# Kernel tuning notes

Hardware: AMD Instinct MI355X
Metric: run time of the kernel (lower is better)

Reference implementation:

```python
import jax, jax.numpy as jnp
import numpy as np

N_NODES = 50000
N_EDGES = 800000
IN_DIM = 256
OUT_DIM = 256


def setup_inputs() -> dict:
    key = jax.random.key(0)
    k_feat, k_src, k_dst, k_w0, k_w1, k_b = jax.random.split(key, 6)
    feat = jax.random.normal(k_feat, (N_NODES, IN_DIM), dtype=jnp.float32)
    src = jax.random.randint(k_src, (N_EDGES,), 0, N_NODES, dtype=jnp.int64)
    dst = jax.random.randint(k_dst, (N_EDGES,), 0, N_NODES, dtype=jnp.int64)
    # GraphConv weights (Glorot-ish scale) and biases
    W0 = jax.random.normal(k_w0, (IN_DIM, OUT_DIM), dtype=jnp.float32) / np.sqrt(IN_DIM)
    W1 = jax.random.normal(k_w1, (OUT_DIM, OUT_DIM), dtype=jnp.float32) / np.sqrt(OUT_DIM)
    b0 = jnp.zeros((OUT_DIM,), dtype=jnp.float32)
    b1 = jnp.zeros((OUT_DIM,), dtype=jnp.float32)
    # single shared nn.PReLU parameter (torch default init 0.25)
    prelu_a = jnp.asarray(0.25, dtype=jnp.float32)
    return {"feat": feat, "src": src, "dst": dst,
            "W0": W0, "b0": b0, "W1": W1, "b1": b1, "prelu_a": prelu_a}


def _prelu(x, a):
    return jnp.where(x >= 0, x, a * x)


def reference(feat, src, dst, W0, b0, W1, b1, prelu_a):
    N = feat.shape[0]
    ones = jnp.ones((src.shape[0],), dtype=feat.dtype)
    out_deg = jnp.zeros((N,), dtype=feat.dtype).at[src].add(ones)
    in_deg = jnp.zeros((N,), dtype=feat.dtype).at[dst].add(ones)
    # DGL norm='both': clamp degrees to >=1 before rsqrt
    norm_s = jax.lax.rsqrt(jnp.maximum(out_deg, 1.0))[:, None]  # [N,1]
    norm_d = jax.lax.rsqrt(jnp.maximum(in_deg, 1.0))[:, None]   # [N,1]

    def graph_conv(h, W, b):
        # h' = D_in^{-1/2} A (D_out^{-1/2} h) W + b
        msg = (h * norm_s)[src]                                   # [E, d]
        agg = jax.ops.segment_sum(msg, dst, num_segments=N)       # [N, d]
        return (agg * norm_d) @ W + b

    h = _prelu(graph_conv(feat, W0, b0), prelu_a)
    hg = jnp.sum(h, axis=0, keepdims=True)                        # SumPooling [1, d]
    h = _prelu(graph_conv(h, W1, b1), prelu_a)
    hg = jnp.concatenate([hg, jnp.sum(h, axis=0, keepdims=True)], axis=-1)
    return (h, hg)
```

## Files before the change

kernel.cpp:

```cpp
#include <hip/hip_runtime.h>
#include <stdint.h>

#define NN 50000
#define NE 800000
#define DIM 256

#define HB 128
#define HT 512
#define HALF 25000

#define NSLICE 4
#define SCH 64
#define NPB 32
#define ECH 1024

#define GR 64
#define GB ((NN + GR - 1) / GR)

#define SCB 49

typedef __bf16 bf16x8 __attribute__((ext_vector_type(8)));
typedef float f32x4 __attribute__((ext_vector_type(4)));
typedef float f32x2 __attribute__((ext_vector_type(2)));
typedef unsigned u32x4 __attribute__((ext_vector_type(4)));
typedef int i32x4 __attribute__((ext_vector_type(4)));

__device__ __forceinline__ unsigned short f2bf(float f) {
  union { float f; unsigned u; } v; v.f = f;
  unsigned r = v.u + 0x7fffu + ((v.u >> 16) & 1u);
  return (unsigned short)(r >> 16);
}

__device__ __forceinline__ void gload_lds16(const void* g, void* l) {
  __builtin_amdgcn_global_load_lds(
      (const __attribute__((address_space(1))) unsigned*)g,
      (__attribute__((address_space(3))) unsigned*)l, 16, 0, 0);
}

__global__ __launch_bounds__(HT) void hist_kernel(const int* __restrict__ src,
                                                  const int* __restrict__ dst,
                                                  unsigned* __restrict__ Hs,
                                                  unsigned* __restrict__ Hd) {
  __shared__ unsigned lds[HALF];
  const int tid = threadIdx.x;
  const int phase = blockIdx.x >> 7;
  const int b = blockIdx.x & (HB - 1);
  const int* arr = phase ? dst : src;
  unsigned* H = phase ? Hd : Hs;
  for (int w = tid; w < HALF; w += HT) lds[w] = 0u;
  __syncthreads();
  for (int e = b * HT + tid; e < NE; e += HB * HT) {
    unsigned n = (unsigned)arr[e];
    atomicAdd(&lds[n >> 1], 1u << ((n & 1) * 16));
  }
  __syncthreads();
  for (int w = tid; w < HALF; w += HT)
    H[(size_t)b * HALF + w] = lds[w];
}

__global__ __launch_bounds__(512) void reduce_norm_kernel(const unsigned* __restrict__ Hs,
                                                          const unsigned* __restrict__ Hd,
                                                          unsigned* __restrict__ Pd,
                                                          int* __restrict__ in_cnt,
                                                          float* __restrict__ norm_s,
                                                          float* __restrict__ norm_d,
                                                          float* __restrict__ hg,
                                                          int* __restrict__ csum) {
  __shared__ int ws[8];
  const int tid = threadIdx.x;
  const int w = blockIdx.x * 512 + tid;
  if (blockIdx.x == 0) hg[tid] = 0.f;
  unsigned ss = 0, dd = 0;
  if (w < HALF) {
    for (int b = 0; b < HB; ++b) {
      Pd[(size_t)b * HALF + w] = dd;
      ss += Hs[(size_t)b * HALF + w];
      dd += Hd[(size_t)b * HALF + w];
    }
    int n0 = w * 2;
    unsigned s0 = ss & 0xffffu, s1 = ss >> 16;
    unsigned d0 = dd & 0xffffu, d1 = dd >> 16;
    in_cnt[n0] = (int)d0;
    in_cnt[n0 + 1] = (int)d1;
    norm_s[n0] = rsqrtf(fmaxf((float)s0, 1.0f));
    norm_s[n0 + 1] = rsqrtf(fmaxf((float)s1, 1.0f));
    norm_d[n0] = rsqrtf(fmaxf((float)d0, 1.0f));
    norm_d[n0 + 1] = rsqrtf(fmaxf((float)d1, 1.0f));
  }
  int deg = (int)((dd & 0xffffu) + (dd >> 16));
  int lane = tid & 63, wave = tid >> 6;
#pragma unroll
  for (int off = 32; off; off >>= 1) deg += __shfl_down(deg, off, 64);
  if (lane == 0) ws[wave] = deg;
  __syncthreads();
  if (tid == 0) {
    int s = 0;
#pragma unroll
    for (int i = 0; i < 8; ++i) s += ws[i];
    csum[blockIdx.x] = s;
  }
}

__global__ __launch_bounds__(256) void scan_write_kernel(const int* __restrict__ in_cnt,
                                                         const int* __restrict__ csum,
                                                         int* __restrict__ row_ptr) {
  __shared__ int wsum[4];
  int tid = threadIdx.x, lane = tid & 63, wave = tid >> 6;
  int cv = (lane < SCB) ? csum[lane] : 0;
  int cincl = cv;
#pragma unroll
  for (int off = 1; off < 64; off <<= 1) {
    int t = __shfl_up(cincl, off, 64);
    if (lane >= off) cincl += t;
  }
  int myoff = __shfl(cincl, blockIdx.x, 64) - __shfl(cv, blockIdx.x, 64);
  int total = __shfl(cincl, SCB - 1, 64);
  if (blockIdx.x == 0 && tid == 0) row_ptr[NN] = total;

  int i0 = blockIdx.x * 1024 + tid * 4;
  int v[4];
#pragma unroll
  for (int j = 0; j < 4; ++j) {
    int i = i0 + j;
    v[j] = (i < NN) ? in_cnt[i] : 0;
  }
  int tsum = v[0] + v[1] + v[2] + v[3];
  int incl = tsum;
#pragma unroll
  for (int off = 1; off < 64; off <<= 1) {
    int t = __shfl_up(incl, off, 64);
    if (lane >= off) incl += t;
  }
  if (lane == 63) wsum[wave] = incl;
  __syncthreads();
  int woff = 0;
  for (int w = 0; w < wave; ++w) woff += wsum[w];
  int run = myoff + woff + (incl - tsum);
#pragma unroll
  for (int j = 0; j < 4; ++j) {
    int i = i0 + j;
    if (i < NN) row_ptr[i] = run;
    run += v[j];
  }
}

__global__ __launch_bounds__(HT) void fill_kernel(const int* __restrict__ src,
                                                  const int* __restrict__ dst,
                                                  const int* __restrict__ row_ptr,
                                                  const unsigned* __restrict__ Pd,
                                                  int* __restrict__ colx) {
  __shared__ unsigned lds[HALF];
  const int tid = threadIdx.x;
  const int b = blockIdx.x;
  for (int w = tid; w < HALF; w += HT) lds[w] = 0u;
  __syncthreads();
  for (int e = b * HT + tid; e < NE; e += HB * HT) {
    int n = dst[e];
    int sh = (n & 1) * 16;
    unsigned old = atomicAdd(&lds[n >> 1], 1u << sh);
    unsigned rank = (old >> sh) & 0xffffu;
    unsigned pref = (Pd[(size_t)b * HALF + (n >> 1)] >> sh) & 0xffffu;
    colx[row_ptr[n] + (int)pref + (int)rank] = src[e] << 7;
  }
}

__device__ __forceinline__ void swizzleW_body(const float* __restrict__ W,
                                              unsigned short* __restrict__ Wb, int idx) {
  int lane = idx & 63;
  int blk = idx >> 6;
  int kc = blk & 7, nt = blk >> 3;
  int kbase = kc * 32 + (lane >> 4) * 8;
  int col = nt * 16 + (lane & 15);
  ushort4 o0, o1;
  o0.x = f2bf(W[(size_t)(kbase + 0) * DIM + col]);
  o0.y = f2bf(W[(size_t)(kbase + 1) * DIM + col]);
  o0.z = f2bf(W[(size_t)(kbase + 2) * DIM + col]);
  o0.w = f2bf(W[(size_t)(kbase + 3) * DIM + col]);
  o1.x = f2bf(W[(size_t)(kbase + 4) * DIM + col]);
  o1.y = f2bf(W[(size_t)(kbase + 5) * DIM + col]);
  o1.z = f2bf(W[(size_t)(kbase + 6) * DIM + col]);
  o1.w = f2bf(W[(size_t)(kbase + 7) * DIM + col]);
  ((ushort4*)Wb)[idx * 2 + 0] = o0;
  ((ushort4*)Wb)[idx * 2 + 1] = o1;
}

__global__ void prep_kernel(const float* __restrict__ feat, const float* __restrict__ norm_s,
                            unsigned short* __restrict__ featb,
                            const float* __restrict__ W0, unsigned short* __restrict__ Wb0,
                            const float* __restrict__ W1, unsigned short* __restrict__ Wb1) {
  int blk = blockIdx.x;
  if (blk < 12500) {
    int i = blk * 256 + threadIdx.x;
    int node = i >> 6;
    int ch4 = i & 63;
    float s = norm_s[node];
    float4 v = ((const float4*)feat)[i];
    ushort4 o;
    o.x = f2bf(v.x * s); o.y = f2bf(v.y * s); o.z = f2bf(v.z * s); o.w = f2bf(v.w * s);
    int sl = ch4 >> 4;
    int w4 = ch4 & 15;
    ((ushort4*)featb)[(size_t)sl * (NN * 16) + (size_t)node * 16 + w4] = o;
  } else if (blk < 12532) {
    swizzleW_body(W0, Wb0, (blk - 12500) * 256 + threadIdx.x);
  } else {
    swizzleW_body(W1, Wb1, (blk - 12532) * 256 + threadIdx.x);
  }
}

__device__ __forceinline__ void acc_row(f32x2* a, u32x4 p) {
  f32x2 v0 = { __uint_as_float(p.x << 16), __uint_as_float(p.x & 0xffff0000u) };
  a[0] += v0;
  f32x2 v1 = { __uint_as_float(p.y << 16), __uint_as_float(p.y & 0xffff0000u) };
  a[1] += v1;
  f32x2 v2 = { __uint_as_float(p.z << 16), __uint_as_float(p.z & 0xffff0000u) };
  a[2] += v2;
  f32x2 v3 = { __uint_as_float(p.w << 16), __uint_as_float(p.w & 0xffff0000u) };
  a[3] += v3;
}

__global__ __launch_bounds__(256) void agg_kernel(const unsigned short* __restrict__ X,
                                                  unsigned short* __restrict__ agg,
                                                  const int* __restrict__ row_ptr,
                                                  const int* __restrict__ colx,
                                                  const float* __restrict__ norm_d) {
  __shared__ int ecol[ECH];
  const int s = blockIdx.x & (NSLICE - 1);
  const int nb = blockIdx.x >> 2;
  const int tid = threadIdx.x;
  const int grp = tid >> 3;
  const int cl = tid & 7;
  const int node = nb * NPB + grp;

  const int nfirst = nb * NPB;
  const int nlast = (nfirst + NPB < NN) ? (nfirst + NPB) : NN;
  const int estart = row_ptr[nfirst];
  const int eend = row_ptr[nlast];

  int e = 0, end = 0;
  if (node < NN) { e = row_ptr[node]; end = row_ptr[node + 1]; }

  const char* Xp = (const char*)(X + (size_t)s * (NN * SCH));
  const int lsub = cl * 16;

  f32x2 a[4];
#pragma unroll
  for (int j = 0; j < 4; ++j) a[j] = (f32x2){0.f, 0.f};

  const int base0 = estart & ~3;
  for (int base = base0; base < eend; base += ECH) {
    const int lim = (base + ECH < eend) ? (base + ECH) : eend;
    __syncthreads();
    for (int k = base + tid * 4; k < lim; k += 1024) {
      i32x4 v = __builtin_nontemporal_load((const i32x4*)(colx + k));
      *(i32x4*)&ecol[k - base] = v;
    }
    __syncthreads();
    const int hi = (end < lim) ? end : lim;
    for (; e + 8 <= hi; e += 8) {
      int o_[8];
#pragma unroll
      for (int j = 0; j < 8; ++j) o_[j] = ecol[e - base + j];
      u32x4 r_[8];
#pragma unroll
      for (int j = 0; j < 8; ++j)
        r_[j] = *(const u32x4*)(Xp + (size_t)(unsigned)(o_[j] | lsub));
#pragma unroll
      for (int j = 0; j < 8; ++j) acc_row(a, r_[j]);
    }
    if (e + 4 <= hi) {
      int o_[4];
#pragma unroll
      for (int j = 0; j < 4; ++j) o_[j] = ecol[e - base + j];
      u32x4 r_[4];
#pragma unroll
      for (int j = 0; j < 4; ++j)
        r_[j] = *(const u32x4*)(Xp + (size_t)(unsigned)(o_[j] | lsub));
#pragma unroll
      for (int j = 0; j < 4; ++j) acc_row(a, r_[j]);
      e += 4;
    }
    for (; e < hi; ++e) {
      int o0 = ecol[e - base];
      u32x4 r = *(const u32x4*)(Xp + (size_t)(unsigned)(o0 | lsub));
      acc_row(a, r);
    }
  }

  if (node < NN) {
    float nd = norm_d[node];
    u32x4 o;
    o.x = (unsigned)f2bf(a[0].x * nd) | ((unsigned)f2bf(a[0].y * nd) << 16);
    o.y = (unsigned)f2bf(a[1].x * nd) | ((unsigned)f2bf(a[1].y * nd) << 16);
    o.z = (unsigned)f2bf(a[2].x * nd) | ((unsigned)f2bf(a[2].y * nd) << 16);
    o.w = (unsigned)f2bf(a[3].x * nd) | ((unsigned)f2bf(a[3].y * nd) << 16);
    unsigned pcol = (unsigned)(s * 128 + cl * 16) ^ (((unsigned)node & 7u) << 4);
    __builtin_nontemporal_store(o, (u32x4*)((char*)agg + (size_t)node * 512 + pcol));
  }
}

#define FROW 260
__global__ __launch_bounds__(256) void gemm_mfma_kernel(const unsigned short* __restrict__ A,
                                                        const unsigned short* __restrict__ Wb,
                                                        const float* __restrict__ bias,
                                                        const float* __restrict__ prelu_a_ptr,
                                                        const float* __restrict__ norm_s,
                                                        float* __restrict__ C,
                                                        unsigned short* __restrict__ Cb,
                                                        float* __restrict__ hg_part) {
  __shared__ __attribute__((aligned(16))) char Asb[GR * 512];
  int tid = threadIdx.x;
  int r0 = blockIdx.x * GR;
  const char* Ab = (const char*)A;
#pragma unroll
  for (int p = 0; p < 8; ++p) {
    int off = p * 4096 + tid * 16;
    int row = off >> 9;
    int col = off & 511;
    int grow = r0 + row;
    if (grow > NN - 1) grow = NN - 1;
    gload_lds16(Ab + (size_t)grow * 512 + col, Asb + off);
  }
  __syncthreads();

  int wave = tid >> 6, lane = tid & 63;
  int quad = lane >> 4, l16 = lane & 15;

  f32x4 acc[4][4];
#pragma unroll
  for (int mt = 0; mt < 4; ++mt)
#pragma unroll
    for (int nti = 0; nti < 4; ++nti)
      acc[mt][nti] = (f32x4){0.f, 0.f, 0.f, 0.f};

#pragma unroll
  for (int kc = 0; kc < 8; ++kc) {
    bf16x8 a[4], b[4];
#pragma unroll
    for (int mt = 0; mt < 4; ++mt) {
      int row = mt * 16 + l16;
      int c = (kc * 64 + quad * 16) ^ ((row & 7) << 4);
      a[mt] = *(const bf16x8*)(Asb + row * 512 + c);
    }
#pragma unroll
    for (int nti = 0; nti < 4; ++nti) {
      int nt = wave * 4 + nti;
      b[nti] = *(const bf16x8*)(Wb + ((size_t)(nt * 8 + kc) * 64 + lane) * 8);
    }
#pragma unroll
    for (int mt = 0; mt < 4; ++mt)
#pragma unroll
      for (int nti = 0; nti < 4; ++nti)
        acc[mt][nti] = __builtin_amdgcn_mfma_f32_16x16x32_bf16(a[mt], b[nti], acc[mt][nti], 0, 0, 0);
  }

  float pa = *prelu_a_ptr;
  float bv[4], cs[4];
#pragma unroll
  for (int nti = 0; nti < 4; ++nti) {
    bv[nti] = bias[wave * 64 + nti * 16 + l16];
    cs[nti] = 0.f;
  }
#pragma unroll
  for (int mt = 0; mt < 4; ++mt) {
#pragma unroll
    for (int nti = 0; nti < 4; ++nti) {
#pragma unroll
      for (int r = 0; r < 4; ++r) {
        int rowg = r0 + mt * 16 + quad * 4 + r;
        float x = acc[mt][nti][r] + bv[nti];
        x = (x >= 0.f) ? x : pa * x;
        acc[mt][nti][r] = x;
        if (rowg < NN) cs[nti] += x;
      }
    }
  }
#pragma unroll
  for (int nti = 0; nti < 4; ++nti) {
    cs[nti] += __shfl_xor(cs[nti], 16, 64);
    cs[nti] += __shfl_xor(cs[nti], 32, 64);
  }
  if (quad == 0) {
#pragma unroll
    for (int nti = 0; nti < 4; ++nti)
      hg_part[(size_t)blockIdx.x * 256 + wave * 64 + nti * 16 + l16] = cs[nti];
  }

  float* LF = (float*)Asb;
#pragma unroll
  for (int chunk = 0; chunk < 4; ++chunk) {
    __syncthreads();
#pragma unroll
    for (int nti = 0; nti < 4; ++nti) {
      int colw = wave * 64 + nti * 16 + l16;
#pragma unroll
      for (int r = 0; r < 4; ++r)
        LF[(quad * 4 + r) * FROW + colw] = acc[chunk][nti][r];
    }
    __syncthreads();
    int rowbase = r0 + chunk * 16;
    if (C) {
#pragma unroll
      for (int s = 0; s < 4; ++s) {
        int g = s * 256 + tid;
        int row = g >> 6, cg = g & 63;
        int rowg = rowbase + row;
        if (rowg < NN) {
          float4 v = *(const float4*)&LF[row * FROW + cg * 4];
          *(float4*)(C + (size_t)rowg * DIM + cg * 4) = v;
        }
      }
    }
    if (Cb) {
#pragma unroll
      for (int s = 0; s < 2; ++s) {
        int g = s * 256 + tid;
        int row = g >> 5, cg = g & 31;
        int rowg = rowbase + row;
        if (rowg < NN) {
          float ns = norm_s[rowg];
          float4 v0 = *(const float4*)&LF[row * FROW + cg * 8];
          float4 v1 = *(const float4*)&LF[row * FROW + cg * 8 + 4];
          uint4 o;
          o.x = (unsigned)f2bf(v0.x * ns) | ((unsigned)f2bf(v0.y * ns) << 16);
          o.y = (unsigned)f2bf(v0.z * ns) | ((unsigned)f2bf(v0.w * ns) << 16);
          o.z = (unsigned)f2bf(v1.x * ns) | ((unsigned)f2bf(v1.y * ns) << 16);
          o.w = (unsigned)f2bf(v1.z * ns) | ((unsigned)f2bf(v1.w * ns) << 16);
          unsigned short* outp = Cb + (size_t)(cg >> 3) * (NN * SCH)
                               + (size_t)rowg * SCH + (size_t)(cg & 7) * 8;
          *(uint4*)outp = o;
        }
      }
    }
  }
}

__global__ __launch_bounds__(256) void hg_reduce_kernel(const float* __restrict__ hg_part,
                                                        float* __restrict__ hg) {
  const int layer = blockIdx.x >> 3;
  const int chunk = blockIdx.x & 7;
  const int c = threadIdx.x;
  const float* base = hg_part + (size_t)layer * GB * 256;
  const int per = (GB + 7) / 8;
  int b0 = chunk * per;
  int b1 = (b0 + per < GB) ? (b0 + per) : GB;
  float s0 = 0.f, s1 = 0.f, s2 = 0.f, s3 = 0.f;
  int b = b0;
  for (; b + 4 <= b1; b += 4) {
    s0 += base[(size_t)(b + 0) * 256 + c];
    s1 += base[(size_t)(b + 1) * 256 + c];
    s2 += base[(size_t)(b + 2) * 256 + c];
    s3 += base[(size_t)(b + 3) * 256 + c];
  }
  for (; b < b1; ++b) s0 += base[(size_t)b * 256 + c];
  atomicAdd(&hg[layer * 256 + c], (s0 + s1) + (s2 + s3));
}

extern "C" void kernel_launch(void* const* d_in, const int* in_sizes, int n_in,
                              void* d_out, int out_size, void* d_ws, size_t ws_size,
                              hipStream_t stream) {
  const float* feat = (const float*)d_in[0];
  const int* src    = (const int*)d_in[1];
  const int* dst    = (const int*)d_in[2];
  const float* W0   = (const float*)d_in[3];
  const float* b0   = (const float*)d_in[4];
  const float* W1   = (const float*)d_in[5];
  const float* b1   = (const float*)d_in[6];
  const float* pa   = (const float*)d_in[7];

  float* out_h = (float*)d_out;
  float* hg    = out_h + (size_t)NN * DIM;

  char* w = (char*)d_ws;
  int* in_cnt   = (int*)w;        w += (size_t)NN * 4;
  float* norm_s = (float*)w;      w += (size_t)NN * 4;
  float* norm_d = (float*)w;      w += (size_t)NN * 4;
  int* row_ptr  = (int*)w;        w += (size_t)(NN + 16) * 4;
  int* colx     = (int*)w;        w += (size_t)(NE + 4) * 4;
  int* csum     = (int*)w;        w += 64 * 4;
  unsigned short* Wb0 = (unsigned short*)w;  w += (size_t)DIM * DIM * 2;
  unsigned short* Wb1 = (unsigned short*)w;  w += (size_t)DIM * DIM * 2;
  float* hg_part = (float*)w;     w += (size_t)2 * GB * 256 * 4;
  uintptr_t ap = ((uintptr_t)w + 255) & ~(uintptr_t)255;
  unsigned short* featb = (unsigned short*)ap;
  unsigned short* aggb  = featb + (size_t)NN * DIM;
  unsigned* Hs = (unsigned*)featb;
  unsigned* Hd = Hs + (size_t)HB * HALF;
  unsigned* Pd = (unsigned*)aggb;

  const int agg_blocks = NSLICE * ((NN + NPB - 1) / NPB);

  hist_kernel<<<2 * HB, HT, 0, stream>>>(src, dst, Hs, Hd);
  reduce_norm_kernel<<<SCB, 512, 0, stream>>>(Hs, Hd, Pd, in_cnt, norm_s, norm_d, hg, csum);
  prep_kernel<<<12564, 256, 0, stream>>>(feat, norm_s, featb, W0, Wb0, W1, Wb1);
  scan_write_kernel<<<SCB, 256, 0, stream>>>(in_cnt, csum, row_ptr);
  fill_kernel<<<HB, HT, 0, stream>>>(src, dst, row_ptr, Pd, colx);

  agg_kernel<<<agg_blocks, 256, 0, stream>>>(featb, aggb, row_ptr, colx, norm_d);
  gemm_mfma_kernel<<<GB, 256, 0, stream>>>(aggb, Wb0, b0, pa, norm_s,
                                           (float*)nullptr, featb, hg_part);

  agg_kernel<<<agg_blocks, 256, 0, stream>>>(featb, aggb, row_ptr, colx, norm_d);
  gemm_mfma_kernel<<<GB, 256, 0, stream>>>(aggb, Wb1, b1, pa, norm_s,
                                           out_h, (unsigned short*)nullptr, hg_part + (size_t)GB * 256);

  hg_reduce_kernel<<<16, 256, 0, stream>>>(hg_part, hg);
}
```

Before: 303.3 us.

## Build CSR with global atomics and aggregate two node groups per block

Drops the per-block LDS histogram and prefix-reduction path that built a deterministic CSR. In its place, a zero kernel, a global-atomic degree count and a global atomic cursor fill colx with edges in nondeterministic order within each row. The aggregation kernel now handles 64 nodes per block (two per thread group) with a larger edge chunk and a 16-wide unrolled gather. The goal is less preprocessing traffic and better latency hiding in the gather. The cost is heavy global atomic contention, and the summation order is no longer deterministic.

Measured after the change: 379.2 us. 1.25x slower.

```diff
diff --git a/kernel.cpp b/kernel.cpp
--- a/kernel.cpp
+++ b/kernel.cpp
@@ -5,14 +5,10 @@
 #define NE 800000
 #define DIM 256
 
-#define HB 128
-#define HT 512
-#define HALF 25000
-
 #define NSLICE 4
 #define SCH 64
-#define NPB 32
-#define ECH 1024
+#define NPB 64
+#define ECH 2048
 
 #define GR 64
 #define GB ((NN + GR - 1) / GR)
@@ -37,75 +33,63 @@
       (__attribute__((address_space(3))) unsigned*)l, 16, 0, 0);
 }
 
-__global__ __launch_bounds__(HT) void hist_kernel(const int* __restrict__ src,
+__global__ __launch_bounds__(256) void zero_kernel(int* __restrict__ cnt, float* __restrict__ hg) {
+  int i = blockIdx.x * 256 + threadIdx.x;
+  if (i < 2 * NN) cnt[i] = 0;
+  if (i < 512) hg[i] = 0.f;
+}
+
+__global__ __launch_bounds__(256) void deg_kernel(const int* __restrict__ src,
                                                   const int* __restrict__ dst,
-                                                  unsigned* __restrict__ Hs,
-                                                  unsigned* __restrict__ Hd) {
-  __shared__ unsigned lds[HALF];
-  const int tid = threadIdx.x;
-  const int phase = blockIdx.x >> 7;
-  const int b = blockIdx.x & (HB - 1);
-  const int* arr = phase ? dst : src;
-  unsigned* H = phase ? Hd : Hs;
-  for (int w = tid; w < HALF; w += HT) lds[w] = 0u;
+                                                  int* __restrict__ cnt) {
+  int t = blockIdx.x * 256 + threadIdx.x;
+  if (t < NE / 4) {
+    i32x4 s4 = *(const i32x4*)(src + t * 4);
+    i32x4 d4 = *(const i32x4*)(dst + t * 4);
+    atomicAdd(&cnt[s4.x], 1);
+    atomicAdd(&cnt[s4.y], 1);
+    atomicAdd(&cnt[s4.z], 1);
+    atomicAdd(&cnt[s4.w], 1);
+    atomicAdd(&cnt[NN + d4.x], 1);
+    atomicAdd(&cnt[NN + d4.y], 1);
+    atomicAdd(&cnt[NN + d4.z], 1);
+    atomicAdd(&cnt[NN + d4.w], 1);
+  }
+}
+
+__global__ __launch_bounds__(256) void norm_kernel(const int* __restrict__ cnt,
+                                                   float* __restrict__ norm_s,
+                                                   float* __restrict__ norm_d,
+                                                   int* __restrict__ csum) {
+  __shared__ int ws[4];
+  int tid = threadIdx.x;
+  int i0 = blockIdx.x * 1024 + tid * 4;
+  int dsum = 0;
+#pragma unroll
+  for (int j = 0; j < 4; ++j) {
+    int i = i0 + j;
+    if (i < NN) {
+      int s = cnt[i], d = cnt[NN + i];
+      norm_s[i] = rsqrtf(fmaxf((float)s, 1.0f));
+      norm_d[i] = rsqrtf(fmaxf((float)d, 1.0f));
+      dsum += d;
+    }
+  }
+  int lane = tid & 63, wave = tid >> 6;
+#pragma unroll
+  for (int off = 32; off; off >>= 1) dsum += __shfl_down(dsum, off, 64);
+  if (lane == 0) ws[wave] = dsum;
   __syncthreads();
-  for (int e = b * HT + tid; e < NE; e += HB * HT) {
-    unsigned n = (unsigned)arr[e];
-    atomicAdd(&lds[n >> 1], 1u << ((n & 1) * 16));
-  }
-  __syncthreads();
-  for (int w = tid; w < HALF; w += HT)
-    H[(size_t)b * HALF + w] = lds[w];
-}
-
-__global__ __launch_bounds__(512) void reduce_norm_kernel(const unsigned* __restrict__ Hs,
-                                                          const unsigned* __restrict__ Hd,
-                                                          unsigned* __restrict__ Pd,
-                                                          int* __restrict__ in_cnt,
-                                                          float* __restrict__ norm_s,
-                                                          float* __restrict__ norm_d,
-                                                          float* __restrict__ hg,
-                                                          int* __restrict__ csum) {
-  __shared__ int ws[8];
-  const int tid = threadIdx.x;
-  const int w = blockIdx.x * 512 + tid;
-  if (blockIdx.x == 0) hg[tid] = 0.f;
-  unsigned ss = 0, dd = 0;
-  if (w < HALF) {
-    for (int b = 0; b < HB; ++b) {
-      Pd[(size_t)b * HALF + w] = dd;
-      ss += Hs[(size_t)b * HALF + w];
-      dd += Hd[(size_t)b * HALF + w];
-    }
-    int n0 = w * 2;
-    unsigned s0 = ss & 0xffffu, s1 = ss >> 16;
-    unsigned d0 = dd & 0xffffu, d1 = dd >> 16;
-    in_cnt[n0] = (int)d0;
-    in_cnt[n0 + 1] = (int)d1;
-    norm_s[n0] = rsqrtf(fmaxf((float)s0, 1.0f));
-    norm_s[n0 + 1] = rsqrtf(fmaxf((float)s1, 1.0f));
-    norm_d[n0] = rsqrtf(fmaxf((float)d0, 1.0f));
-    norm_d[n0 + 1] = rsqrtf(fmaxf((float)d1, 1.0f));
-  }
-  int deg = (int)((dd & 0xffffu) + (dd >> 16));
-  int lane = tid & 63, wave = tid >> 6;
-#pragma unroll
-  for (int off = 32; off; off >>= 1) deg += __shfl_down(deg, off, 64);
-  if (lane == 0) ws[wave] = deg;
-  __syncthreads();
-  if (tid == 0) {
-    int s = 0;
-#pragma unroll
-    for (int i = 0; i < 8; ++i) s += ws[i];
-    csum[blockIdx.x] = s;
-  }
-}
-
-__global__ __launch_bounds__(256) void scan_write_kernel(const int* __restrict__ in_cnt,
+  if (tid == 0) csum[blockIdx.x] = ws[0] + ws[1] + ws[2] + ws[3];
+}
+
+__global__ __launch_bounds__(256) void scan_write_kernel(const int* __restrict__ cnt,
                                                          const int* __restrict__ csum,
-                                                         int* __restrict__ row_ptr) {
+                                                         int* __restrict__ row_ptr,
+                                                         int* __restrict__ cur) {
   __shared__ int wsum[4];
   int tid = threadIdx.x, lane = tid & 63, wave = tid >> 6;
+  const int* in_cnt = cnt + NN;
   int cv = (lane < SCB) ? csum[lane] : 0;
   int cincl = cv;
 #pragma unroll
@@ -139,28 +123,27 @@
 #pragma unroll
   for (int j = 0; j < 4; ++j) {
     int i = i0 + j;
-    if (i < NN) row_ptr[i] = run;
+    if (i < NN) { row_ptr[i] = run; cur[i] = run; }
     run += v[j];
   }
 }
 
-__global__ __launch_bounds__(HT) void fill_kernel(const int* __restrict__ src,
-                                                  const int* __restrict__ dst,
-                                                  const int* __restrict__ row_ptr,
-                                                  const unsigned* __restrict__ Pd,
-                                                  int* __restrict__ colx) {
-  __shared__ unsigned lds[HALF];
-  const int tid = threadIdx.x;
-  const int b = blockIdx.x;
-  for (int w = tid; w < HALF; w += HT) lds[w] = 0u;
-  __syncthreads();
-  for (int e = b * HT + tid; e < NE; e += HB * HT) {
-    int n = dst[e];
-    int sh = (n & 1) * 16;
-    unsigned old = atomicAdd(&lds[n >> 1], 1u << sh);
-    unsigned rank = (old >> sh) & 0xffffu;
-    unsigned pref = (Pd[(size_t)b * HALF + (n >> 1)] >> sh) & 0xffffu;
-    colx[row_ptr[n] + (int)pref + (int)rank] = src[e] << 7;
+__global__ __launch_bounds__(256) void fill_kernel(const int* __restrict__ src,
+                                                   const int* __restrict__ dst,
+                                                   int* __restrict__ cur,
+                                                   int* __restrict__ colx) {
+  int t = blockIdx.x * 256 + threadIdx.x;
+  if (t < NE / 4) {
+    i32x4 s4 = *(const i32x4*)(src + t * 4);
+    i32x4 d4 = *(const i32x4*)(dst + t * 4);
+    int p0 = atomicAdd(&cur[d4.x], 1);
+    colx[p0] = s4.x << 7;
+    int p1 = atomicAdd(&cur[d4.y], 1);
+    colx[p1] = s4.y << 7;
+    int p2 = atomicAdd(&cur[d4.z], 1);
+    colx[p2] = s4.z << 7;
+    int p3 = atomicAdd(&cur[d4.w], 1);
+    colx[p3] = s4.w << 7;
   }
 }
 
@@ -229,72 +212,104 @@
   const int tid = threadIdx.x;
   const int grp = tid >> 3;
   const int cl = tid & 7;
-  const int node = nb * NPB + grp;
 
   const int nfirst = nb * NPB;
   const int nlast = (nfirst + NPB < NN) ? (nfirst + NPB) : NN;
   const int estart = row_ptr[nfirst];
   const int eend = row_ptr[nlast];
 
-  int e = 0, end = 0;
-  if (node < NN) { e = row_ptr[node]; end = row_ptr[node + 1]; }
-
   const char* Xp = (const char*)(X + (size_t)s * (NN * SCH));
   const int lsub = cl * 16;
 
-  f32x2 a[4];
-#pragma unroll
-  for (int j = 0; j < 4; ++j) a[j] = (f32x2){0.f, 0.f};
+  int nodes[2];
+  nodes[0] = nfirst + grp;
+  nodes[1] = nfirst + 32 + grp;
+
+  f32x2 acc2[2][4];
+#pragma unroll
+  for (int q = 0; q < 2; ++q)
+#pragma unroll
+    for (int j = 0; j < 4; ++j) acc2[q][j] = (f32x2){0.f, 0.f};
+
+  int e_[2], end_[2];
+#pragma unroll
+  for (int q = 0; q < 2; ++q) {
+    if (nodes[q] < NN) { e_[q] = row_ptr[nodes[q]]; end_[q] = row_ptr[nodes[q] + 1]; }
+    else { e_[q] = 0; end_[q] = 0; }
+  }
 
   const int base0 = estart & ~3;
   for (int base = base0; base < eend; base += ECH) {
     const int lim = (base + ECH < eend) ? (base + ECH) : eend;
     __syncthreads();
     for (int k = base + tid * 4; k < lim; k += 1024) {
-      i32x4 v = __builtin_nontemporal_load((const i32x4*)(colx + k));
+      i32x4 v = *(const i32x4*)(colx + k);
       *(i32x4*)&ecol[k - base] = v;
     }
     __syncthreads();
-    const int hi = (end < lim) ? end : lim;
-    for (; e + 8 <= hi; e += 8) {
-      int o_[8];
-#pragma unroll
-      for (int j = 0; j < 8; ++j) o_[j] = ecol[e - base + j];
-      u32x4 r_[8];
-#pragma unroll
-      for (int j = 0; j < 8; ++j)
-        r_[j] = *(const u32x4*)(Xp + (size_t)(unsigned)(o_[j] | lsub));
-#pragma unroll
-      for (int j = 0; j < 8; ++j) acc_row(a, r_[j]);
-    }
-    if (e + 4 <= hi) {
-      int o_[4];
-#pragma unroll
-      for (int j = 0; j < 4; ++j) o_[j] = ecol[e - base + j];
-      u32x4 r_[4];
-#pragma unroll
-      for (int j = 0; j < 4; ++j)
-        r_[j] = *(const u32x4*)(Xp + (size_t)(unsigned)(o_[j] | lsub));
-#pragma unroll
-      for (int j = 0; j < 4; ++j) acc_row(a, r_[j]);
-      e += 4;
-    }
-    for (; e < hi; ++e) {
-      int o0 = ecol[e - base];
-      u32x4 r = *(const u32x4*)(Xp + (size_t)(unsigned)(o0 | lsub));
-      acc_row(a, r);
-    }
-  }
-
-  if (node < NN) {
-    float nd = norm_d[node];
-    u32x4 o;
-    o.x = (unsigned)f2bf(a[0].x * nd) | ((unsigned)f2bf(a[0].y * nd) << 16);
-    o.y = (unsigned)f2bf(a[1].x * nd) | ((unsigned)f2bf(a[1].y * nd) << 16);
-    o.z = (unsigned)f2bf(a[2].x * nd) | ((unsigned)f2bf(a[2].y * nd) << 16);
-    o.w = (unsigned)f2bf(a[3].x * nd) | ((unsigned)f2bf(a[3].y * nd) << 16);
-    unsigned pcol = (unsigned)(s * 128 + cl * 16) ^ (((unsigned)node & 7u) << 4);
-    __builtin_nontemporal_store(o, (u32x4*)((char*)agg + (size_t)node * 512 + pcol));
+#pragma unroll
+    for (int q = 0; q < 2; ++q) {
+      int e = e_[q];
+      const int hi = (end_[q] < lim) ? end_[q] : lim;
+      f32x2* a = acc2[q];
+      for (; e + 16 <= hi; e += 16) {
+        int o_[16];
+#pragma unroll
+        for (int j = 0; j < 16; ++j) o_[j] = ecol[e - base + j];
+        u32x4 r_[16];
+#pragma unroll
+        for (int j = 0; j < 16; ++j)
+          r_[j] = *(const u32x4*)(Xp + (size_t)(unsigned)(o_[j] | lsub));
+#pragma unroll
+        for (int j = 0; j < 16; ++j) acc_row(a, r_[j]);
+      }
+      if (e + 8 <= hi) {
+        int o_[8];
+#pragma unroll
+        for (int j = 0; j < 8; ++j) o_[j] = ecol[e - base + j];
+        u32x4 r_[8];
+#pragma unroll
+        for (int j = 0; j < 8; ++j)
+          r_[j] = *(const u32x4*)(Xp + (size_t)(unsigned)(o_[j] | lsub));
+#pragma unroll
+        for (int j = 0; j < 8; ++j) acc_row(a, r_[j]);
+        e += 8;
+      }
+      if (e + 4 <= hi) {
+        int o_[4];
+#pragma unroll
+        for (int j = 0; j < 4; ++j) o_[j] = ecol[e - base + j];
+        u32x4 r_[4];
+#pragma unroll
+        for (int j = 0; j < 4; ++j)
+          r_[j] = *(const u32x4*)(Xp + (size_t)(unsigned)(o_[j] | lsub));
+#pragma unroll
+        for (int j = 0; j < 4; ++j) acc_row(a, r_[j]);
+        e += 4;
+      }
+      for (; e < hi; ++e) {
+        int o0 = ecol[e - base];
+        u32x4 r = *(const u32x4*)(Xp + (size_t)(unsigned)(o0 | lsub));
+        acc_row(a, r);
+      }
+      e_[q] = e;
+    }
+  }
+
+#pragma unroll
+  for (int q = 0; q < 2; ++q) {
+    int node = nodes[q];
+    if (node < NN) {
+      float nd = norm_d[node];
+      f32x2* a = acc2[q];
+      u32x4 o;
+      o.x = (unsigned)f2bf(a[0].x * nd) | ((unsigned)f2bf(a[0].y * nd) << 16);
+      o.y = (unsigned)f2bf(a[1].x * nd) | ((unsigned)f2bf(a[1].y * nd) << 16);
+      o.z = (unsigned)f2bf(a[2].x * nd) | ((unsigned)f2bf(a[2].y * nd) << 16);
+      o.w = (unsigned)f2bf(a[3].x * nd) | ((unsigned)f2bf(a[3].y * nd) << 16);
+      unsigned pcol = (unsigned)(s * 128 + cl * 16) ^ (((unsigned)node & 7u) << 4);
+      __builtin_nontemporal_store(o, (u32x4*)((char*)agg + (size_t)node * 512 + pcol));
+    }
   }
 }
 
@@ -471,10 +486,11 @@
   float* hg    = out_h + (size_t)NN * DIM;
 
   char* w = (char*)d_ws;
-  int* in_cnt   = (int*)w;        w += (size_t)NN * 4;
+  int* cnt      = (int*)w;        w += (size_t)2 * NN * 4;
   float* norm_s = (float*)w;      w += (size_t)NN * 4;
   float* norm_d = (float*)w;      w += (size_t)NN * 4;
   int* row_ptr  = (int*)w;        w += (size_t)(NN + 16) * 4;
+  int* cur      = (int*)w;        w += (size_t)NN * 4;
   int* colx     = (int*)w;        w += (size_t)(NE + 4) * 4;
   int* csum     = (int*)w;        w += 64 * 4;
   unsigned short* Wb0 = (unsigned short*)w;  w += (size_t)DIM * DIM * 2;
@@ -483,17 +499,15 @@
   uintptr_t ap = ((uintptr_t)w + 255) & ~(uintptr_t)255;
   unsigned short* featb = (unsigned short*)ap;
   unsigned short* aggb  = featb + (size_t)NN * DIM;
-  unsigned* Hs = (unsigned*)featb;
-  unsigned* Hd = Hs + (size_t)HB * HALF;
-  unsigned* Pd = (unsigned*)aggb;
 
   const int agg_blocks = NSLICE * ((NN + NPB - 1) / NPB);
 
-  hist_kernel<<<2 * HB, HT, 0, stream>>>(src, dst, Hs, Hd);
-  reduce_norm_kernel<<<SCB, 512, 0, stream>>>(Hs, Hd, Pd, in_cnt, norm_s, norm_d, hg, csum);
+  zero_kernel<<<(2 * NN + 255) / 256, 256, 0, stream>>>(cnt, hg);
+  deg_kernel<<<(NE / 4 + 255) / 256, 256, 0, stream>>>(src, dst, cnt);
+  norm_kernel<<<SCB, 256, 0, stream>>>(cnt, norm_s, norm_d, csum);
   prep_kernel<<<12564, 256, 0, stream>>>(feat, norm_s, featb, W0, Wb0, W1, Wb1);
-  scan_write_kernel<<<SCB, 256, 0, stream>>>(in_cnt, csum, row_ptr);
-  fill_kernel<<<HB, HT, 0, stream>>>(src, dst, row_ptr, Pd, colx);
+  scan_write_kernel<<<SCB, 256, 0, stream>>>(cnt, csum, row_ptr, cur);
+  fill_kernel<<<(NE / 4 + 255) / 256, 256, 0, stream>>>(src, dst, cur, colx);
 
   agg_kernel<<<agg_blocks, 256, 0, stream>>>(featb, aggb, row_ptr, colx, norm_d);
   gemm_mfma_kernel<<<GB, 256, 0, stream>>>(aggb, Wb0, b0, pa, norm_s,
```

## Process two destination nodes per thread group in aggregation kernel

Applied to the files above, without the earlier changes.

Each block of the aggregation kernel now covers 64 destination nodes instead of 32, and each 8-thread group walks two nodes in turn. The shared edge-index staging buffer doubles to 2048 entries, and the inner gather loop is unrolled to 16 rows. The column-index load also switches from a nontemporal load to a normal one. The aim is to cut per-block overhead, halve the grid, and keep more gather loads in flight, at the cost of more registers and LDS per block and so possibly lower occupancy.

Measured after the change: 302.1 us. About the same (-0.4%).

```diff
diff --git a/kernel.cpp b/kernel.cpp
--- a/kernel.cpp
+++ b/kernel.cpp
@@ -11,8 +11,8 @@
 
 #define NSLICE 4
 #define SCH 64
-#define NPB 32
-#define ECH 1024
+#define NPB 64
+#define ECH 2048
 
 #define GR 64
 #define GB ((NN + GR - 1) / GR)
@@ -229,72 +229,104 @@
   const int tid = threadIdx.x;
   const int grp = tid >> 3;
   const int cl = tid & 7;
-  const int node = nb * NPB + grp;
 
   const int nfirst = nb * NPB;
   const int nlast = (nfirst + NPB < NN) ? (nfirst + NPB) : NN;
   const int estart = row_ptr[nfirst];
   const int eend = row_ptr[nlast];
 
-  int e = 0, end = 0;
-  if (node < NN) { e = row_ptr[node]; end = row_ptr[node + 1]; }
-
   const char* Xp = (const char*)(X + (size_t)s * (NN * SCH));
   const int lsub = cl * 16;
 
-  f32x2 a[4];
-#pragma unroll
-  for (int j = 0; j < 4; ++j) a[j] = (f32x2){0.f, 0.f};
+  int nodes[2];
+  nodes[0] = nfirst + grp;
+  nodes[1] = nfirst + 32 + grp;
+
+  f32x2 acc2[2][4];
+#pragma unroll
+  for (int q = 0; q < 2; ++q)
+#pragma unroll
+    for (int j = 0; j < 4; ++j) acc2[q][j] = (f32x2){0.f, 0.f};
+
+  int e_[2], end_[2];
+#pragma unroll
+  for (int q = 0; q < 2; ++q) {
+    if (nodes[q] < NN) { e_[q] = row_ptr[nodes[q]]; end_[q] = row_ptr[nodes[q] + 1]; }
+    else { e_[q] = 0; end_[q] = 0; }
+  }
 
   const int base0 = estart & ~3;
   for (int base = base0; base < eend; base += ECH) {
     const int lim = (base + ECH < eend) ? (base + ECH) : eend;
     __syncthreads();
     for (int k = base + tid * 4; k < lim; k += 1024) {
-      i32x4 v = __builtin_nontemporal_load((const i32x4*)(colx + k));
+      i32x4 v = *(const i32x4*)(colx + k);
       *(i32x4*)&ecol[k - base] = v;
     }
     __syncthreads();
-    const int hi = (end < lim) ? end : lim;
-    for (; e + 8 <= hi; e += 8) {
-      int o_[8];
-#pragma unroll
-      for (int j = 0; j < 8; ++j) o_[j] = ecol[e - base + j];
-      u32x4 r_[8];
-#pragma unroll
-      for (int j = 0; j < 8; ++j)
-        r_[j] = *(const u32x4*)(Xp + (size_t)(unsigned)(o_[j] | lsub));
-#pragma unroll
-      for (int j = 0; j < 8; ++j) acc_row(a, r_[j]);
-    }
-    if (e + 4 <= hi) {
-      int o_[4];
-#pragma unroll
-      for (int j = 0; j < 4; ++j) o_[j] = ecol[e - base + j];
-      u32x4 r_[4];
-#pragma unroll
-      for (int j = 0; j < 4; ++j)
-        r_[j] = *(const u32x4*)(Xp + (size_t)(unsigned)(o_[j] | lsub));
-#pragma unroll
-      for (int j = 0; j < 4; ++j) acc_row(a, r_[j]);
-      e += 4;
-    }
-    for (; e < hi; ++e) {
-      int o0 = ecol[e - base];
-      u32x4 r = *(const u32x4*)(Xp + (size_t)(unsigned)(o0 | lsub));
-      acc_row(a, r);
-    }
-  }
-
-  if (node < NN) {
-    float nd = norm_d[node];
-    u32x4 o;
-    o.x = (unsigned)f2bf(a[0].x * nd) | ((unsigned)f2bf(a[0].y * nd) << 16);
-    o.y = (unsigned)f2bf(a[1].x * nd) | ((unsigned)f2bf(a[1].y * nd) << 16);
-    o.z = (unsigned)f2bf(a[2].x * nd) | ((unsigned)f2bf(a[2].y * nd) << 16);
-    o.w = (unsigned)f2bf(a[3].x * nd) | ((unsigned)f2bf(a[3].y * nd) << 16);
-    unsigned pcol = (unsigned)(s * 128 + cl * 16) ^ (((unsigned)node & 7u) << 4);
-    __builtin_nontemporal_store(o, (u32x4*)((char*)agg + (size_t)node * 512 + pcol));
+#pragma unroll
+    for (int q = 0; q < 2; ++q) {
+      int e = e_[q];
+      const int hi = (end_[q] < lim) ? end_[q] : lim;
+      f32x2* a = acc2[q];
+      for (; e + 16 <= hi; e += 16) {
+        int o_[16];
+#pragma unroll
+        for (int j = 0; j < 16; ++j) o_[j] = ecol[e - base + j];
+        u32x4 r_[16];
+#pragma unroll
+        for (int j = 0; j < 16; ++j)
+          r_[j] = *(const u32x4*)(Xp + (size_t)(unsigned)(o_[j] | lsub));
+#pragma unroll
+        for (int j = 0; j < 16; ++j) acc_row(a, r_[j]);
+      }
+      if (e + 8 <= hi) {
+        int o_[8];
+#pragma unroll
+        for (int j = 0; j < 8; ++j) o_[j] = ecol[e - base + j];
+        u32x4 r_[8];
+#pragma unroll
+        for (int j = 0; j < 8; ++j)
+          r_[j] = *(const u32x4*)(Xp + (size_t)(unsigned)(o_[j] | lsub));
+#pragma unroll
+        for (int j = 0; j < 8; ++j) acc_row(a, r_[j]);
+        e += 8;
+      }
+      if (e + 4 <= hi) {
+        int o_[4];
+#pragma unroll
+        for (int j = 0; j < 4; ++j) o_[j] = ecol[e - base + j];
+        u32x4 r_[4];
+#pragma unroll
+        for (int j = 0; j < 4; ++j)
+          r_[j] = *(const u32x4*)(Xp + (size_t)(unsigned)(o_[j] | lsub));
+#pragma unroll
+        for (int j = 0; j < 4; ++j) acc_row(a, r_[j]);
+        e += 4;
+      }
+      for (; e < hi; ++e) {
+        int o0 = ecol[e - base];
+        u32x4 r = *(const u32x4*)(Xp + (size_t)(unsigned)(o0 | lsub));
+        acc_row(a, r);
+      }
+      e_[q] = e;
+    }
+  }
+
+#pragma unroll
+  for (int q = 0; q < 2; ++q) {
+    int node = nodes[q];
+    if (node < NN) {
+      float nd = norm_d[node];
+      f32x2* a = acc2[q];
+      u32x4 o;
+      o.x = (unsigned)f2bf(a[0].x * nd) | ((unsigned)f2bf(a[0].y * nd) << 16);
+      o.y = (unsigned)f2bf(a[1].x * nd) | ((unsigned)f2bf(a[1].y * nd) << 16);
+      o.z = (unsigned)f2bf(a[2].x * nd) | ((unsigned)f2bf(a[2].y * nd) << 16);
+      o.w = (unsigned)f2bf(a[3].x * nd) | ((unsigned)f2bf(a[3].y * nd) << 16);
+      unsigned pcol = (unsigned)(s * 128 + cl * 16) ^ (((unsigned)node & 7u) << 4);
+      __builtin_nontemporal_store(o, (u32x4*)((char*)agg + (size_t)node * 512 + pcol));
+    }
   }
 }
 
```
